# Kernel tuning notes

Measured on AMD Instinct MI355X. Metric: run time of the kernel, lower is better.

The kernel has to match this reference:

```python
import jax, jax.numpy as jnp
import numpy as np

# Module-level constants (GRID_SIZE and anchor count from the original repo's globals)
GH, GW = 52, 52          # GRID_SIZE = [H, W]
A = 9                    # number of anchors
G = GH * GW              # flattened grid cells
L_COOR_OBJ = L_COOR_NOOBJ = L_CONF_OBJ = L_CONF_NOOBJ = 1.0


def setup_inputs() -> dict:
    key = jax.random.key(0)
    k1, k2, k3 = jax.random.split(key, 3)
    pred = jax.random.normal(k1, (256, G, A, 5), dtype=jnp.float32)
    # normalized xywh labels, kept away from the borders so boxes are sane
    label = jax.random.uniform(k2, (256, 4), dtype=jnp.float32, minval=0.05, maxval=0.95)
    anchors = jax.random.uniform(k3, (A, 2), dtype=jnp.float32, minval=0.05, maxval=0.6)
    return {"pred": pred, "label": label, "anchors": anchors}


def _clip_corners(cxy, wh):
    # [N,4] -> clipped (x1,y1,x2,y2), matching the torch max/min with 0/1
    x1 = jnp.maximum(cxy[:, 0] - wh[:, 0] / 2, 0.0)
    y1 = jnp.maximum(cxy[:, 1] - wh[:, 1] / 2, 0.0)
    x2 = jnp.minimum(cxy[:, 0] + wh[:, 0] / 2, 1.0)
    y2 = jnp.minimum(cxy[:, 1] + wh[:, 1] / 2, 1.0)
    return jnp.stack([x1, y1, x2, y2], axis=1)


def _forward(pred_raw, label, anchors):
    B = pred_raw.shape[0]
    flat = jnp.arange(G)
    cx = (flat // GH).astype(jnp.float32)   # x-major flat ordering: flat = x*GH + y
    cy = (flat % GH).astype(jnp.float32)

    # --- YOLOout decode: xy = (sigmoid + cell)/grid, wh = anchors*exp, conf = sigmoid ---
    x = (jax.nn.sigmoid(pred_raw[..., 0]) + cx[None, :, None]) / GW      # [B,G,A]
    y = (jax.nn.sigmoid(pred_raw[..., 1]) + cy[None, :, None]) / GH
    wh = anchors[None, None] * jnp.exp(pred_raw[..., 2:4])               # [B,G,A,2]
    conf = jax.nn.sigmoid(pred_raw[..., 4])                              # [B,G,A]
    pred = jnp.concatenate([x[..., None], y[..., None], wh, conf[..., None]], axis=-1)

    # --- responsible cell / anchor indices ---
    idx_x = jnp.floor(label[:, 0] * GW)
    idx_y = jnp.floor(label[:, 1] * GH)
    idx = (idx_x * GH + idx_y).astype(jnp.int32)                         # [B]
    # NOTE: original uses argmax of squared distance (faithful, even if odd)
    anchor_mask = jnp.argmax(
        jnp.sum((label[:, None, 2:4] - anchors[None]) ** 2, axis=-1), axis=1
    )                                                                    # [B]

    # --- anchors_grid [G,A,4]: cell-center xy + anchor wh ---
    ag_x = jnp.broadcast_to(((cx + 0.5) / GW)[:, None], (G, A))
    ag_y = jnp.broadcast_to(((cy + 0.5) / GH)[:, None], (G, A))
    ag_wh = jnp.broadcast_to(anchors[None], (G, A, 2))
    anchors_grid = jnp.concatenate([ag_x[..., None], ag_y[..., None], ag_wh], axis=-1)

    # --- gather the single responsible prediction per sample ---
    b_idx = jnp.arange(B)
    pred_obj = pred[b_idx, idx, anchor_mask]          # [B,5]
    ag_obj = anchors_grid[idx, anchor_mask]           # [B,4]

    # --- noobj MSE = (sum over all) - (sum over obj entries), static shapes ---
    GA1 = G * A - 1
    coor_sq_all = jnp.sum((pred[..., :4] - anchors_grid[None]) ** 2)
    coor_sq_obj = jnp.sum((pred_obj[:, :4] - ag_obj) ** 2)
    coor_l_noobj = (coor_sq_all - coor_sq_obj) / (B * GA1 * 4)
    conf_l_noobj = (jnp.sum(conf ** 2) - jnp.sum(pred_obj[:, 4] ** 2)) / (B * GA1)

    # --- IoU between gathered obj boxes and labels (argmax over a single box is identity) ---
    label_bb = _clip_corners(label[:, :2], label[:, 2:4])
    pred_bb = _clip_corners(pred_obj[:, :2], pred_obj[:, 2:4])
    ix1 = jnp.maximum(label_bb[:, 0], pred_bb[:, 0])
    iy1 = jnp.maximum(label_bb[:, 1], pred_bb[:, 1])
    ix2 = jnp.minimum(label_bb[:, 2], pred_bb[:, 2])
    iy2 = jnp.minimum(label_bb[:, 3], pred_bb[:, 3])
    # faithful to original: areas computed as x2*y2 (not (x2-x1)*(y2-y1))
    label_area = label_bb[:, 2] * label_bb[:, 3]
    pred_area = pred_bb[:, 2] * pred_bb[:, 3]
    inter_area = jnp.maximum(ix2 - ix1, 0.0) * jnp.maximum(iy2 - iy1, 0.0)
    iou = inter_area / (label_area + pred_area - inter_area)

    coor_l_obj = jnp.mean((pred_obj[:, :4] - label) ** 2)
    conf_l_obj = jnp.mean((pred_obj[:, 4] - iou) ** 2)

    return (coor_l_obj * L_COOR_OBJ + coor_l_noobj * L_COOR_NOOBJ
            + conf_l_obj * L_CONF_OBJ + conf_l_noobj * L_CONF_NOOBJ)


def reference(pred, label, anchors):
    return _forward(pred, label, anchors)
```

## Files before the change

### kernel.cpp

```cpp
#include <hip/hip_runtime.h>


#define GHW     52
#define GCELLS  2704
#define NA      9
#define BATCH   256
#define NBLK    (GCELLS * NA)
#define INV52   (1.0f / 52.0f)
#define NBUCKET 256

__device__ __forceinline__ float sigmoidf_(float x) {
    return 1.0f / (1.0f + __expf(-x));
}

__device__ __forceinline__ float waveReduceSum(float v) {
#pragma unroll
    for (int o = 32; o > 0; o >>= 1) v += __shfl_down(v, o, 64);
    return v;
}

__global__ __launch_bounds__(256) void yolo_obj_kernel(
        const float* __restrict__ pred,
        const float* __restrict__ label,
        const float* __restrict__ anchors,
        float* __restrict__ ws) {
    __shared__ float anch[18];
    __shared__ float red[4][4];
    int b = threadIdx.x;
    if (b < 18) anch[b] = anchors[b];
    __syncthreads();

    float4 lab = ((const float4*)label)[b];
    float lx = lab.x, ly = lab.y, lw = lab.z, lh = lab.w;

    int ix = (int)floorf(lx * 52.0f);
    int iy = (int)floorf(ly * 52.0f);
    int idx = ix * GHW + iy;

    int am = 0; float best = -1.0f;
#pragma unroll
    for (int a = 0; a < NA; ++a) {
        float dw = lw - anch[2 * a];
        float dh = lh - anch[2 * a + 1];
        float d = dw * dw + dh * dh;
        if (d > best) { best = d; am = a; }
    }

    const float* p = pred + (((size_t)b * GCELLS + idx) * NA + am) * 5;
    float v0 = p[0], v1 = p[1], v2 = p[2], v3 = p[3], v4 = p[4];

    float aw = anch[2 * am], ah = anch[2 * am + 1];
    float px = (sigmoidf_(v0) + (float)ix) * INV52;
    float py = (sigmoidf_(v1) + (float)iy) * INV52;
    float pw = aw * __expf(v2);
    float ph = ah * __expf(v3);
    float pc = sigmoidf_(v4);

    float agx = ((float)ix + 0.5f) * INV52;
    float agy = ((float)iy + 0.5f) * INV52;

    float d0 = px - agx, d1 = py - agy, d2 = pw - aw, d3 = ph - ah;
    float coor_sq_obj = d0 * d0 + d1 * d1 + d2 * d2 + d3 * d3;
    float conf_sq_obj = pc * pc;

    float e0 = px - lx, e1 = py - ly, e2 = pw - lw, e3 = ph - lh;
    float coor_obj = e0 * e0 + e1 * e1 + e2 * e2 + e3 * e3;

    float lx1 = fmaxf(lx - lw * 0.5f, 0.0f), ly1 = fmaxf(ly - lh * 0.5f, 0.0f);
    float lx2 = fminf(lx + lw * 0.5f, 1.0f), ly2 = fminf(ly + lh * 0.5f, 1.0f);
    float qx1 = fmaxf(px - pw * 0.5f, 0.0f), qy1 = fmaxf(py - ph * 0.5f, 0.0f);
    float qx2 = fminf(px + pw * 0.5f, 1.0f), qy2 = fminf(py + ph * 0.5f, 1.0f);
    float ix1 = fmaxf(lx1, qx1), iy1 = fmaxf(ly1, qy1);
    float ix2 = fminf(lx2, qx2), iy2 = fminf(ly2, qy2);
    float la = lx2 * ly2, pa = qx2 * qy2;
    float inter = fmaxf(ix2 - ix1, 0.0f) * fmaxf(iy2 - iy1, 0.0f);
    float iou = inter / (la + pa - inter);
    float dcf = pc - iou;
    float conf_obj = dcf * dcf;

    float r0 = waveReduceSum(coor_sq_obj);
    float r1 = waveReduceSum(conf_sq_obj);
    float r2 = waveReduceSum(coor_obj);
    float r3 = waveReduceSum(conf_obj);
    int lane = threadIdx.x & 63, wid = threadIdx.x >> 6;
    if (lane == 0) {
        red[0][wid] = r0; red[1][wid] = r1; red[2][wid] = r2; red[3][wid] = r3;
    }
    __syncthreads();
    if (threadIdx.x < 4) {
        ws[threadIdx.x] = red[threadIdx.x][0] + red[threadIdx.x][1]
                        + red[threadIdx.x][2] + red[threadIdx.x][3];
    }
}

__global__ __launch_bounds__(256) void yolo_noobj_kernel(
        const float* __restrict__ pred,
        const float* __restrict__ anchors,
        float* __restrict__ ws) {
    __shared__ float sh[1280];
    __shared__ float anch[18];
    __shared__ float red[2][4];
    int t = threadIdx.x;

    size_t f0 = (size_t)blockIdx.x * 320;
    const float4* g4 = (const float4*)pred;
    ((float4*)sh)[t] = g4[f0 + t];
    if (t < 64) ((float4*)sh)[256 + t] = g4[f0 + 256 + t];
    if (t < 18) anch[t] = anchors[t];
    __syncthreads();

    int e = blockIdx.x * 256 + t;
    int a = e % NA;
    float aw = anch[2 * a], ah = anch[2 * a + 1];

    const float* m = sh + 5 * t;
    float v0 = m[0], v1 = m[1], v2 = m[2], v3 = m[3], v4 = m[4];

    float s0 = sigmoidf_(v0);
    float s1 = sigmoidf_(v1);
    float s4 = sigmoidf_(v4);
    float t0 = (s0 - 0.5f) * INV52;
    float t1 = (s1 - 0.5f) * INV52;
    float t2 = aw * (__expf(v2) - 1.0f);
    float t3 = ah * (__expf(v3) - 1.0f);

    float coor = t0 * t0 + t1 * t1 + t2 * t2 + t3 * t3;
    float conf = s4 * s4;

    float rc = waveReduceSum(coor);
    float rf = waveReduceSum(conf);
    int lane = t & 63, wid = t >> 6;
    if (lane == 0) { red[0][wid] = rc; red[1][wid] = rf; }
    __syncthreads();
    if (t == 0) {
        float cs = red[0][0] + red[0][1] + red[0][2] + red[0][3];
        float fs = red[1][0] + red[1][1] + red[1][2] + red[1][3];
        int bk = blockIdx.x & (NBUCKET - 1);
        atomicAdd(&ws[4 + bk], cs);
        atomicAdd(&ws[4 + NBUCKET + bk], fs);
    }
}

__global__ __launch_bounds__(256) void yolo_fin_kernel(
        const float* __restrict__ ws,
        float* __restrict__ out) {
    __shared__ float red[2][4];
    int t = threadIdx.x;
    float c = ws[4 + t];
    float f = ws[4 + NBUCKET + t];
    float rc = waveReduceSum(c);
    float rf = waveReduceSum(f);
    int lane = t & 63, wid = t >> 6;
    if (lane == 0) { red[0][wid] = rc; red[1][wid] = rf; }
    __syncthreads();
    if (t == 0) {
        float coor_all = red[0][0] + red[0][1] + red[0][2] + red[0][3];
        float conf_all = red[1][0] + red[1][1] + red[1][2] + red[1][3];
        float coor_l_noobj = (coor_all - ws[0]) / (float)(BATCH * (NBLK - 1) * 4);
        float conf_l_noobj = (conf_all - ws[1]) / (float)(BATCH * (NBLK - 1));
        float coor_l_obj = ws[2] / (float)(BATCH * 4);
        float conf_l_obj = ws[3] / (float)BATCH;
        out[0] = coor_l_obj + coor_l_noobj + conf_l_obj + conf_l_noobj;
    }
}

extern "C" void kernel_launch(void* const* d_in, const int* in_sizes, int n_in,
                              void* d_out, int out_size, void* d_ws, size_t ws_size,
                              hipStream_t stream) {
    const float* pred    = (const float*)d_in[0];
    const float* label   = (const float*)d_in[1];
    const float* anchors = (const float*)d_in[2];
    float* out = (float*)d_out;
    float* ws  = (float*)d_ws;

    hipMemsetAsync(d_ws, 0, (4 + 2 * NBUCKET) * sizeof(float), stream);

    yolo_obj_kernel<<<1, 256, 0, stream>>>(pred, label, anchors, ws);
    yolo_noobj_kernel<<<NBLK, 256, 0, stream>>>(pred, anchors, ws);
    yolo_fin_kernel<<<1, 256, 0, stream>>>(ws, out);
}
```

Before: 187.0 us.

## Fuse finalize into noobj kernel with last-block reduction and bigger per-thread work

Removes the memset and the separate finalize kernel. The obj kernel now zeroes the workspace, and the last noobj block, found through an atomic counter, does the final reduction. Each thread now handles 8 anchor entries through direct float4 loads instead of staging through shared memory, and the grid shrinks from 24336 blocks to 3042. The sigmoid switches to a hardware reciprocal, trading a little accuracy for fewer launches and less per-block overhead.

Result: slower. 322.7 us (+72.6%).

```diff
diff --git a/kernel.cpp b/kernel.cpp
--- a/kernel.cpp
+++ b/kernel.cpp
@@ -8,9 +8,15 @@
 #define NBLK    (GCELLS * NA)
 #define INV52   (1.0f / 52.0f)
 #define NBUCKET 256
-
-__device__ __forceinline__ float sigmoidf_(float x) {
+#define NB2     3042
+#define CNT_IDX (4 + 2 * NBUCKET)
+
+__device__ __forceinline__ float sigmoid_exact(float x) {
     return 1.0f / (1.0f + __expf(-x));
+}
+
+__device__ __forceinline__ float sigmoid_fast(float x) {
+    return __builtin_amdgcn_rcpf(1.0f + __expf(-x));
 }
 
 __device__ __forceinline__ float waveReduceSum(float v) {
@@ -27,6 +33,11 @@
     __shared__ float anch[18];
     __shared__ float red[4][4];
     int b = threadIdx.x;
+
+    ws[4 + b] = 0.0f;
+    ws[4 + NBUCKET + b] = 0.0f;
+    if (b == 0) ((int*)ws)[CNT_IDX] = 0;
+
     if (b < 18) anch[b] = anchors[b];
     __syncthreads();
 
@@ -50,11 +61,11 @@
     float v0 = p[0], v1 = p[1], v2 = p[2], v3 = p[3], v4 = p[4];
 
     float aw = anch[2 * am], ah = anch[2 * am + 1];
-    float px = (sigmoidf_(v0) + (float)ix) * INV52;
-    float py = (sigmoidf_(v1) + (float)iy) * INV52;
+    float px = (sigmoid_exact(v0) + (float)ix) * INV52;
+    float py = (sigmoid_exact(v1) + (float)iy) * INV52;
     float pw = aw * __expf(v2);
     float ph = ah * __expf(v3);
-    float pc = sigmoidf_(v4);
+    float pc = sigmoid_exact(v4);
 
     float agx = ((float)ix + 0.5f) * INV52;
     float agy = ((float)iy + 0.5f) * INV52;
@@ -96,39 +107,51 @@
 __global__ __launch_bounds__(256) void yolo_noobj_kernel(
         const float* __restrict__ pred,
         const float* __restrict__ anchors,
-        float* __restrict__ ws) {
-    __shared__ float sh[1280];
+        float* __restrict__ ws,
+        float* __restrict__ out) {
     __shared__ float anch[18];
     __shared__ float red[2][4];
+    __shared__ int isLast;
     int t = threadIdx.x;
-
-    size_t f0 = (size_t)blockIdx.x * 320;
-    const float4* g4 = (const float4*)pred;
-    ((float4*)sh)[t] = g4[f0 + t];
-    if (t < 64) ((float4*)sh)[256 + t] = g4[f0 + 256 + t];
     if (t < 18) anch[t] = anchors[t];
     __syncthreads();
 
-    int e = blockIdx.x * 256 + t;
-    int a = e % NA;
-    float aw = anch[2 * a], ah = anch[2 * a + 1];
-
-    const float* m = sh + 5 * t;
-    float v0 = m[0], v1 = m[1], v2 = m[2], v3 = m[3], v4 = m[4];
-
-    float s0 = sigmoidf_(v0);
-    float s1 = sigmoidf_(v1);
-    float s4 = sigmoidf_(v4);
-    float t0 = (s0 - 0.5f) * INV52;
-    float t1 = (s1 - 0.5f) * INV52;
-    float t2 = aw * (__expf(v2) - 1.0f);
-    float t3 = ah * (__expf(v3) - 1.0f);
-
-    float coor = t0 * t0 + t1 * t1 + t2 * t2 + t3 * t3;
-    float conf = s4 * s4;
-
-    float rc = waveReduceSum(coor);
-    float rf = waveReduceSum(conf);
+    const float4* __restrict__ g4 = (const float4*)pred;
+    float coorAcc = 0.0f, confAcc = 0.0f;
+
+#pragma unroll
+    for (int it = 0; it < 2; ++it) {
+        int task = blockIdx.x * 512 + it * 256 + t;
+        size_t fb = (size_t)task * 5;
+        float4 q0 = g4[fb + 0];
+        float4 q1 = g4[fb + 1];
+        float4 q2 = g4[fb + 2];
+        float4 q3 = g4[fb + 3];
+        float4 q4 = g4[fb + 4];
+        float v[20] = {q0.x, q0.y, q0.z, q0.w,
+                       q1.x, q1.y, q1.z, q1.w,
+                       q2.x, q2.y, q2.z, q2.w,
+                       q3.x, q3.y, q3.z, q3.w,
+                       q4.x, q4.y, q4.z, q4.w};
+        int a = (task * 4) % NA;
+#pragma unroll
+        for (int j = 0; j < 4; ++j) {
+            float aw = anch[2 * a], ah = anch[2 * a + 1];
+            float s0 = sigmoid_fast(v[5 * j + 0]);
+            float s1 = sigmoid_fast(v[5 * j + 1]);
+            float s4 = sigmoid_fast(v[5 * j + 4]);
+            float t0 = (s0 - 0.5f) * INV52;
+            float t1 = (s1 - 0.5f) * INV52;
+            float t2 = aw * (__expf(v[5 * j + 2]) - 1.0f);
+            float t3 = ah * (__expf(v[5 * j + 3]) - 1.0f);
+            coorAcc += t0 * t0 + t1 * t1 + t2 * t2 + t3 * t3;
+            confAcc += s4 * s4;
+            a = (a == NA - 1) ? 0 : a + 1;
+        }
+    }
+
+    float rc = waveReduceSum(coorAcc);
+    float rf = waveReduceSum(confAcc);
     int lane = t & 63, wid = t >> 6;
     if (lane == 0) { red[0][wid] = rc; red[1][wid] = rf; }
     __syncthreads();
@@ -138,29 +161,28 @@
         int bk = blockIdx.x & (NBUCKET - 1);
         atomicAdd(&ws[4 + bk], cs);
         atomicAdd(&ws[4 + NBUCKET + bk], fs);
-    }
-}
-
-__global__ __launch_bounds__(256) void yolo_fin_kernel(
-        const float* __restrict__ ws,
-        float* __restrict__ out) {
-    __shared__ float red[2][4];
-    int t = threadIdx.x;
-    float c = ws[4 + t];
-    float f = ws[4 + NBUCKET + t];
-    float rc = waveReduceSum(c);
-    float rf = waveReduceSum(f);
-    int lane = t & 63, wid = t >> 6;
-    if (lane == 0) { red[0][wid] = rc; red[1][wid] = rf; }
-    __syncthreads();
-    if (t == 0) {
-        float coor_all = red[0][0] + red[0][1] + red[0][2] + red[0][3];
-        float conf_all = red[1][0] + red[1][1] + red[1][2] + red[1][3];
-        float coor_l_noobj = (coor_all - ws[0]) / (float)(BATCH * (NBLK - 1) * 4);
-        float conf_l_noobj = (conf_all - ws[1]) / (float)(BATCH * (NBLK - 1));
-        float coor_l_obj = ws[2] / (float)(BATCH * 4);
-        float conf_l_obj = ws[3] / (float)BATCH;
-        out[0] = coor_l_obj + coor_l_noobj + conf_l_obj + conf_l_noobj;
+        __threadfence();
+        int old = atomicAdd((int*)ws + CNT_IDX, 1);
+        isLast = (old == NB2 - 1);
+    }
+    __syncthreads();
+
+    if (isLast) {
+        float c = atomicAdd(&ws[4 + t], 0.0f);
+        float f = atomicAdd(&ws[4 + NBUCKET + t], 0.0f);
+        float rc2 = waveReduceSum(c);
+        float rf2 = waveReduceSum(f);
+        if (lane == 0) { red[0][wid] = rc2; red[1][wid] = rf2; }
+        __syncthreads();
+        if (t == 0) {
+            float coor_all = red[0][0] + red[0][1] + red[0][2] + red[0][3];
+            float conf_all = red[1][0] + red[1][1] + red[1][2] + red[1][3];
+            float coor_l_noobj = (coor_all - ws[0]) / (float)(BATCH * (NBLK - 1) * 4);
+            float conf_l_noobj = (conf_all - ws[1]) / (float)(BATCH * (NBLK - 1));
+            float coor_l_obj = ws[2] / (float)(BATCH * 4);
+            float conf_l_obj = ws[3] / (float)BATCH;
+            out[0] = coor_l_obj + coor_l_noobj + conf_l_obj + conf_l_noobj;
+        }
     }
 }
 
@@ -173,9 +195,6 @@
     float* out = (float*)d_out;
     float* ws  = (float*)d_ws;
 
-    hipMemsetAsync(d_ws, 0, (4 + 2 * NBUCKET) * sizeof(float), stream);
-
     yolo_obj_kernel<<<1, 256, 0, stream>>>(pred, label, anchors, ws);
-    yolo_noobj_kernel<<<NBLK, 256, 0, stream>>>(pred, anchors, ws);
-    yolo_fin_kernel<<<1, 256, 0, stream>>>(ws, out);
-}
+    yolo_noobj_kernel<<<NB2, 256, 0, stream>>>(pred, anchors, ws, out);
+}
```

## Process two elements per thread, drop memset, use fast reciprocal sigmoid

Applied to the files above, without the earlier changes.

The noobj kernel now has each thread handle two elements, which halves the block count and the number of bucket atomics. The separate memset launch is removed, and the obj kernel zeroes the accumulation buckets instead, relying on stream ordering before the noobj kernel runs. The sigmoid in the hot loop uses the hardware approximate reciprocal, which trades a little accuracy for fewer instructions. The workload is bandwidth-bound, so the main savings are one fewer launch and less per-block overhead.

Measured after the change: 182.9 us. 1.02x faster.

```diff
diff --git a/kernel.cpp b/kernel.cpp
--- a/kernel.cpp
+++ b/kernel.cpp
@@ -9,8 +9,16 @@
 #define INV52   (1.0f / 52.0f)
 #define NBUCKET 256
 
-__device__ __forceinline__ float sigmoidf_(float x) {
+#define ELEMS_B 512
+#define NB2     12168
+#define Q4_B    640
+
+__device__ __forceinline__ float sigmoid_exact(float x) {
     return 1.0f / (1.0f + __expf(-x));
+}
+
+__device__ __forceinline__ float sigmoid_fast(float x) {
+    return __builtin_amdgcn_rcpf(1.0f + __expf(-x));
 }
 
 __device__ __forceinline__ float waveReduceSum(float v) {
@@ -27,6 +35,10 @@
     __shared__ float anch[18];
     __shared__ float red[4][4];
     int b = threadIdx.x;
+
+    ws[4 + b] = 0.0f;
+    ws[4 + NBUCKET + b] = 0.0f;
+
     if (b < 18) anch[b] = anchors[b];
     __syncthreads();
 
@@ -50,11 +62,11 @@
     float v0 = p[0], v1 = p[1], v2 = p[2], v3 = p[3], v4 = p[4];
 
     float aw = anch[2 * am], ah = anch[2 * am + 1];
-    float px = (sigmoidf_(v0) + (float)ix) * INV52;
-    float py = (sigmoidf_(v1) + (float)iy) * INV52;
+    float px = (sigmoid_exact(v0) + (float)ix) * INV52;
+    float py = (sigmoid_exact(v1) + (float)iy) * INV52;
     float pw = aw * __expf(v2);
     float ph = ah * __expf(v3);
-    float pc = sigmoidf_(v4);
+    float pc = sigmoid_exact(v4);
 
     float agx = ((float)ix + 0.5f) * INV52;
     float agy = ((float)iy + 0.5f) * INV52;
@@ -97,38 +109,44 @@
         const float* __restrict__ pred,
         const float* __restrict__ anchors,
         float* __restrict__ ws) {
-    __shared__ float sh[1280];
+    __shared__ float sh[ELEMS_B * 5];
     __shared__ float anch[18];
     __shared__ float red[2][4];
     int t = threadIdx.x;
 
-    size_t f0 = (size_t)blockIdx.x * 320;
-    const float4* g4 = (const float4*)pred;
-    ((float4*)sh)[t] = g4[f0 + t];
-    if (t < 64) ((float4*)sh)[256 + t] = g4[f0 + 256 + t];
+    size_t f0 = (size_t)blockIdx.x * Q4_B;
+    const float4* __restrict__ g4 = (const float4*)pred;
+    ((float4*)sh)[t]       = g4[f0 + t];
+    ((float4*)sh)[t + 256] = g4[f0 + 256 + t];
+    if (t < 128) ((float4*)sh)[t + 512] = g4[f0 + 512 + t];
     if (t < 18) anch[t] = anchors[t];
     __syncthreads();
 
-    int e = blockIdx.x * 256 + t;
-    int a = e % NA;
-    float aw = anch[2 * a], ah = anch[2 * a + 1];
+    float coorAcc = 0.0f, confAcc = 0.0f;
+#pragma unroll
+    for (int h = 0; h < 2; ++h) {
+        int le = t + h * 256;
+        int e  = blockIdx.x * ELEMS_B + le;
+        int a  = e % NA;
+        float aw = anch[2 * a], ah = anch[2 * a + 1];
 
-    const float* m = sh + 5 * t;
-    float v0 = m[0], v1 = m[1], v2 = m[2], v3 = m[3], v4 = m[4];
+        const float* m = sh + 5 * le;
+        float v0 = m[0], v1 = m[1], v2 = m[2], v3 = m[3], v4 = m[4];
 
-    float s0 = sigmoidf_(v0);
-    float s1 = sigmoidf_(v1);
-    float s4 = sigmoidf_(v4);
-    float t0 = (s0 - 0.5f) * INV52;
-    float t1 = (s1 - 0.5f) * INV52;
-    float t2 = aw * (__expf(v2) - 1.0f);
-    float t3 = ah * (__expf(v3) - 1.0f);
+        float s0 = sigmoid_fast(v0);
+        float s1 = sigmoid_fast(v1);
+        float s4 = sigmoid_fast(v4);
+        float t0 = (s0 - 0.5f) * INV52;
+        float t1 = (s1 - 0.5f) * INV52;
+        float t2 = aw * (__expf(v2) - 1.0f);
+        float t3 = ah * (__expf(v3) - 1.0f);
 
-    float coor = t0 * t0 + t1 * t1 + t2 * t2 + t3 * t3;
-    float conf = s4 * s4;
+        coorAcc += t0 * t0 + t1 * t1 + t2 * t2 + t3 * t3;
+        confAcc += s4 * s4;
+    }
 
-    float rc = waveReduceSum(coor);
-    float rf = waveReduceSum(conf);
+    float rc = waveReduceSum(coorAcc);
+    float rf = waveReduceSum(confAcc);
     int lane = t & 63, wid = t >> 6;
     if (lane == 0) { red[0][wid] = rc; red[1][wid] = rf; }
     __syncthreads();
@@ -173,9 +191,7 @@
     float* out = (float*)d_out;
     float* ws  = (float*)d_ws;
 
-    hipMemsetAsync(d_ws, 0, (4 + 2 * NBUCKET) * sizeof(float), stream);
-
     yolo_obj_kernel<<<1, 256, 0, stream>>>(pred, label, anchors, ws);
-    yolo_noobj_kernel<<<NBLK, 256, 0, stream>>>(pred, anchors, ws);
+    yolo_noobj_kernel<<<NB2, 256, 0, stream>>>(pred, anchors, ws);
     yolo_fin_kernel<<<1, 256, 0, stream>>>(ws, out);
 }
```
